# Performance work log

Hardware: AMD Instinct MI355X
Metric: run time of the kernel (lower is better)

The kernel has to match this reference:

```python
import jax, jax.numpy as jnp
import numpy as np

N_NODES = 307
U = 100          # gru units / GAT out dim
D_IN = 3         # per-node input features
F_IN = U + D_IN  # 103, GATv2 input dim
NEG_SLOPE = 0.2


def setup_inputs() -> dict:
    key = jax.random.key(0)
    ks = jax.random.split(key, 12)
    B, E = 256, 4096
    inputs = jax.random.normal(ks[0], (B, N_NODES * D_IN), dtype=jnp.float32)
    state = jax.random.normal(ks[1], (B, N_NODES * U), dtype=jnp.float32)
    src = jax.random.randint(ks[2], (E,), 0, N_NODES, dtype=jnp.int32)
    dst = jax.random.randint(ks[3], (E,), 0, N_NODES, dtype=jnp.int32)
    def glorot(k, shape):
        lim = float(np.sqrt(6.0 / (shape[0] + shape[1])))
        return jax.random.uniform(k, shape, jnp.float32, -lim, lim)
    return {
        "inputs": inputs, "state": state, "src": src, "dst": dst,
        "Wl": glorot(ks[4], (F_IN, U)),        # GATv2 lin_l (source)
        "Wr": glorot(ks[5], (F_IN, U)),        # GATv2 lin_r (target)
        "att": jax.random.normal(ks[6], (U,), jnp.float32) * 0.1,
        "gat_bias": jnp.zeros((U,), jnp.float32),
        "bias_gc": jnp.zeros((U,), jnp.float32),   # self.bias_1 added in _gc3
        "W_gru1": glorot(ks[7], (F_IN, 2 * U)),    # GRULinear(100,200)
        "b_gru1": jnp.zeros((2 * U,), jnp.float32),
        "W_gru2": glorot(ks[8], (F_IN, U)),        # GRULinear(100,100)
        "b_gru2": jnp.zeros((U,), jnp.float32),
    }


def _gru_linear(inputs, hidden, W, b):
    # cat((inputs[B,N,3], hidden[B,N,U]), -1) @ W + b
    B = hidden.shape[0]
    x = jnp.concatenate([inputs.reshape(B, N_NODES, D_IN),
                         hidden.reshape(B, N_NODES, U)], axis=2)
    return jnp.einsum('bnf,fo->bno', x, W) + b


def _gatv2(x, src, dst, Wl, Wr, att, gat_bias):
    # x: (B, N, F_IN); PyG GATv2Conv with heads=1, add_self_loops=True
    loops = jnp.arange(N_NODES, dtype=src.dtype)
    s = jnp.concatenate([src, loops])
    d = jnp.concatenate([dst, loops])
    xl = jnp.einsum('bnf,fu->bnu', x, Wl)  # source transform
    xr = jnp.einsum('bnf,fu->bnu', x, Wr)  # target transform

    def per_sample(xl_b, xr_b):
        m = xl_b[s]                                        # (E', U)
        e = jax.nn.leaky_relu(m + xr_b[d], NEG_SLOPE) @ att  # (E',)
        emax = jax.ops.segment_max(e, d, num_segments=N_NODES)
        ex = jnp.exp(e - emax[d])
        denom = jax.ops.segment_sum(ex, d, num_segments=N_NODES)
        alpha = ex / denom[d]
        return jax.ops.segment_sum(alpha[:, None] * m, d, num_segments=N_NODES)

    out = jax.vmap(per_sample)(xl, xr)  # (B, N, U)
    return out + gat_bias


def reference(inputs, state, src, dst, Wl, Wr, att, gat_bias, bias_gc,
              W_gru1, b_gru1, W_gru2, b_gru2):
    B = state.shape[0]
    # _gc3: cat([state, inputs]) -> GATv2 per sample -> + bias_1
    x = jnp.concatenate([state.reshape(B, N_NODES, U),
                         inputs.reshape(B, N_NODES, D_IN)], axis=2)
    st = _gatv2(x, src, dst, Wl, Wr, att, gat_bias) + bias_gc
    st = st.reshape(B, N_NODES * U)
    # GRU gating
    value = jax.nn.sigmoid(_gru_linear(inputs, st, W_gru1, b_gru1))  # (B,N,2U)
    r, u = jnp.split(value, 2, axis=-1)
    r = r.reshape(B, N_NODES * U)
    u = u.reshape(B, N_NODES * U)
    c = jnp.tanh(_gru_linear(inputs, r * st, W_gru2, b_gru2)).reshape(B, N_NODES * U)
    return u * st + (1.0 - u) * c
```

## Files before the change

kernel.cpp:

```cpp
#include <hip/hip_runtime.h>
#include <math.h>

#define NN 307
#define UU 100
#define DD 3
#define UP 104
#define UNIT_W 14336
#define HCAP 2560
#define NT 512
#define NGRP (NT / 16)

typedef _Float16 f16;
typedef f16  f16x2 __attribute__((ext_vector_type(2)));
typedef f16  f16x4 __attribute__((ext_vector_type(4)));
typedef f16  f16x8 __attribute__((ext_vector_type(8)));
typedef float f32x4 __attribute__((ext_vector_type(4)));
typedef unsigned short u16;

__global__ __launch_bounds__(256)
void pack_w_k(const float* __restrict__ Wl, const float* __restrict__ Wr,
              const float* __restrict__ Wg1, const float* __restrict__ Wg2,
              f16* __restrict__ Wp)
{
    const int idx = blockIdx.x * 256 + threadIdx.x;
    const int u   = idx / UNIT_W;
    const int rem = idx - u * UNIT_W;
    const int e   = rem & 7;
    const int l   = (rem >> 3) & 63;
    const int sj  = rem >> 9;
    const int s   = sj / 7, j = sj - 7 * s;
    const int col = j * 16 + (l & 15);
    const int k   = (s * 4 + (l >> 4)) * 8 + e;
    float v = 0.f;
    if (col < UU && k < UU + DD) {
        if (u == 0)      v = Wl[k * UU + col];
        else if (u == 1) v = Wr[k * UU + col];
        else {
            const int kk = (k < UU) ? (k + DD) : (k - UU);
            if (u == 2)      v = Wg1[kk * (2 * UU) + col];
            else if (u == 3) v = Wg1[kk * (2 * UU) + UU + col];
            else             v = Wg2[kk * UU + col];
        }
    }
    Wp[idx] = (f16)v;
}

__global__ __launch_bounds__(64)
void csr_count_k(const int* __restrict__ dst, int E, int* offs)
{
    const int d = blockIdx.x;
    const int lane = threadIdx.x;
    const int Etot = E + NN;
    int c = 0;
    for (int base = 0; base < Etot; base += 64) {
        const int e = base + lane;
        if (e < Etot) {
            const int de = (e < E) ? dst[e] : (e - E);
            c += (de == d) ? 1 : 0;
        }
    }
    #pragma unroll
    for (int m = 1; m < 64; m <<= 1) c += __shfl_xor(c, m, 64);
    if (lane == 0) {
        offs[d + 1] = c;
        if (d == 0) offs[0] = 0;
    }
}

__global__ __launch_bounds__(512)
void csr_scan_k(int* offs)
{
    __shared__ int c[512];
    const int t = threadIdx.x;
    c[t] = (t < NN) ? offs[t + 1] : 0;
    __syncthreads();
    #pragma unroll
    for (int off = 1; off < 512; off <<= 1) {
        const int v = (t >= off) ? c[t - off] : 0;
        __syncthreads();
        c[t] += v;
        __syncthreads();
    }
    if (t < NN) offs[t + 1] = c[t];
    if (t == 0) offs[0] = 0;
}

__global__ __launch_bounds__(64)
void csr_fill_k(const int* __restrict__ src, const int* __restrict__ dst,
                int E, const int* __restrict__ offs,
                int* eidx, int* ddst)
{
    const int d = blockIdx.x;
    const int lane = threadIdx.x;
    const int Etot = E + NN;
    int w = offs[d];
    for (int base = 0; base < Etot; base += 64) {
        const int e = base + lane;
        bool match = false;
        int se = 0;
        if (e < Etot) {
            const int de = (e < E) ? dst[e] : (e - E);
            se           = (e < E) ? src[e] : (e - E);
            match = (de == d);
        }
        const unsigned long long mask = __ballot(match);
        if (match) {
            const int pos = w + __popcll(mask & ((1ULL << lane) - 1ULL));
            eidx[pos] = se;
            ddst[pos] = d;
        }
        w += __popcll(mask);
    }
}

__device__ __forceinline__ void mma_unit_nb(const f16x8 (&af)[4],
                                            const f16* __restrict__ Wu,
                                            int l, f32x4 (&acc)[7])
{
    #pragma unroll
    for (int s = 0; s < 4; ++s)
        #pragma unroll
        for (int j = 0; j < 7; ++j) {
            const f16x8 bv = *(const f16x8*)(Wu + (((s * 7 + j) * 64 + l) << 3));
            acc[j] = __builtin_amdgcn_mfma_f32_16x16x32_f16(af[s], bv, acc[j], 0, 0, 0);
        }
}

__device__ __forceinline__ void z7(f32x4 (&acc)[7])
{
    #pragma unroll
    for (int j = 0; j < 7; ++j) acc[j] = (f32x4)0.f;
}

__device__ __forceinline__ float fast_sigmoid(float x)
{
    return __fdividef(1.f, 1.f + __expf(-x));
}

__device__ __forceinline__ float fast_tanh(float x)
{
    return 1.f - __fdividef(2.f, __expf(2.f * x) + 1.f);
}

__global__ __launch_bounds__(256, 4)
void gemm_xlxr_k(const float* __restrict__ state, const float* __restrict__ inp,
                 const f16* __restrict__ Wp,
                 f16* __restrict__ xl, f16* __restrict__ xr, int M)
{
    const int tid = threadIdx.x;
    const int w = tid >> 6, l = tid & 63, lr = l & 15, lk = l >> 4;
    const int rb = blockIdx.x * 64 + w * 16;
    int crow = rb + lr; if (crow >= M) crow = M - 1;
    const float* bf = state + (size_t)crow * UU;

    f16x8 af[4];
    #pragma unroll
    for (int s = 0; s < 3; ++s) {
        const int kb = s * 4 + lk;
        const float4 x0 = *(const float4*)(bf + kb * 8);
        const float4 x1 = *(const float4*)(bf + kb * 8 + 4);
        f16x8 v;
        v[0]=(f16)x0.x; v[1]=(f16)x0.y; v[2]=(f16)x0.z; v[3]=(f16)x0.w;
        v[4]=(f16)x1.x; v[5]=(f16)x1.y; v[6]=(f16)x1.z; v[7]=(f16)x1.w;
        af[s] = v;
    }
    {
        f16x8 v = (f16x8)(f16)0.f;
        if (lk == 0) {
            const float4 x0 = *(const float4*)(bf + 96);
            v[0]=(f16)x0.x; v[1]=(f16)x0.y; v[2]=(f16)x0.z; v[3]=(f16)x0.w;
            v[4] = (f16)inp[(size_t)crow * DD + 0];
            v[5] = (f16)inp[(size_t)crow * DD + 1];
            v[6] = (f16)inp[(size_t)crow * DD + 2];
            v[7] = (f16)0.f;
        }
        af[3] = v;
    }

    #pragma unroll
    for (int u = 0; u < 2; ++u) {
        f32x4 acc[7];
        z7(acc);
        mma_unit_nb(af, Wp + (size_t)u * UNIT_W, l, acc);
        f16* dst = u ? xr : xl;
        #pragma unroll
        for (int j = 0; j < 7; ++j) {
            const int col = j * 16 + lr;
            if (col >= UU) continue;
            #pragma unroll
            for (int r = 0; r < 4; ++r) {
                const int row = rb + lk * 4 + r;
                if (row < M) dst[(size_t)row * UP + col] = (f16)acc[j][r];
            }
        }
    }
}

__global__ __launch_bounds__(NT)
__attribute__((amdgpu_waves_per_eu(4, 4)))
void gat2h_k(const f16* __restrict__ xl, const f16* __restrict__ xr,
             const int* __restrict__ offs, const int* __restrict__ eidx,
             const int* __restrict__ ddst,
             const float* __restrict__ att, const float* __restrict__ gb,
             const float* __restrict__ bgc,
             f16* __restrict__ stg)
{
    __shared__ f16   xl_s[NN * UP];
    __shared__ float sc_s[HCAP];
    __shared__ u16   ei_s[HCAP];
    __shared__ f16   att_s[UP];

    const int b   = blockIdx.x;
    const int h   = blockIdx.y;
    const int tid = threadIdx.x;
    const int d0 = h * 154;
    const int d1 = (h == 0) ? 154 : NN;
    const f16* xlb = xl + (size_t)b * NN * UP;
    const f16* xrb = xr + (size_t)b * NN * UP;
    f16* stb = stg + (size_t)b * NN * UP;

    if (tid < UP) att_s[tid] = (tid < UU) ? (f16)att[tid] : (f16)0.f;
    for (int c = tid; c < NN * UP / 8; c += NT)
        *(f16x8*)&xl_s[c * 8] = *(const f16x8*)&xlb[c * 8];

    int dlo = d0;
    while (dlo < d1) {
        int dhi = d1;
        const int base = offs[dlo];
        if (offs[d1] - base > HCAP) {
            int lo = dlo + 1, hi = d1;
            while (lo < hi) {
                const int mid = (lo + hi + 1) >> 1;
                if (offs[mid] - base <= HCAP) lo = mid; else hi = mid - 1;
            }
            dhi = lo;
        }
        const int e0 = base, e1 = offs[dhi];
        const int n  = e1 - e0;

        for (int q = tid; q < n; q += NT) ei_s[q] = (u16)eidx[e0 + q];
        __syncthreads();

        for (int i = tid; i < n; i += NT) {
            const int s = ei_s[i];
            const int d = ddst[e0 + i];
            const f16x8* a8 = (const f16x8*)&xl_s[s * UP];
            const f16x8* r8 = (const f16x8*)(xrb + (size_t)d * UP);
            float p0 = 0.f, p1 = 0.f;
            #pragma unroll 4
            for (int c = 0; c < 13; ++c) {
                const f16x8 x  = a8[c] + r8[c];
                const f16x8 xm = x * (f16)0.2f;
                const f16x8 y  = __builtin_elementwise_max(x, xm);
                const f16x2* y2  = (const f16x2*)&y;
                const f16x2* at2 = (const f16x2*)&att_s[c * 8];
#if __has_builtin(__builtin_amdgcn_fdot2)
                p0 = __builtin_amdgcn_fdot2(y2[0], at2[0], p0, false);
                p1 = __builtin_amdgcn_fdot2(y2[1], at2[1], p1, false);
                p0 = __builtin_amdgcn_fdot2(y2[2], at2[2], p0, false);
                p1 = __builtin_amdgcn_fdot2(y2[3], at2[3], p1, false);
#else
                #pragma unroll
                for (int q = 0; q < 4; ++q) {
                    p0 += (float)y2[q][0] * (float)at2[q][0];
                    p1 += (float)y2[q][1] * (float)at2[q][1];
                }
#endif
            }
            sc_s[i] = p0 + p1;
        }
        __syncthreads();

        {
            const int t = dlo + tid;
            if (t < dhi) {
                const int f0 = offs[t] - e0, f1 = offs[t + 1] - e0;
                float mx = -1e30f;
                for (int e = f0; e < f1; ++e) mx = fmaxf(mx, sc_s[e]);
                float dn = 0.f;
                for (int e = f0; e < f1; ++e) {
                    const float ex = __expf(sc_s[e] - mx);
                    sc_s[e] = ex;
                    dn += ex;
                }
                const float inv = 1.f / dn;
                for (int e = f0; e < f1; ++e) sc_s[e] *= inv;
            }
        }
        __syncthreads();

        {
            const int g   = tid >> 4;
            const int sub = tid & 15;
            const bool fa = (sub < 13);
            float bias_r[8];
            #pragma unroll
            for (int k = 0; k < 8; ++k) {
                const int f = sub * 8 + k;
                bias_r[k] = (fa && f < UU) ? (gb[f] + bgc[f]) : 0.f;
            }
            for (int d = dlo + g; d < dhi; d += NGRP) {
                const int f0 = offs[d] - e0, f1 = offs[d + 1] - e0;
                float acc[8] = {0.f, 0.f, 0.f, 0.f, 0.f, 0.f, 0.f, 0.f};
                for (int e = f0; e < f1; ++e) {
                    const float alpha = sc_s[e];
                    const int s = ei_s[e];
                    if (fa) {
                        const f16x8 m = *(const f16x8*)&xl_s[s * UP + sub * 8];
                        #pragma unroll
                        for (int k = 0; k < 8; ++k) acc[k] += alpha * (float)m[k];
                    }
                }
                if (fa) {
                    f16x8 o;
                    #pragma unroll
                    for (int k = 0; k < 8; ++k) o[k] = (f16)(acc[k] + bias_r[k]);
                    *(f16x8*)(stb + (size_t)d * UP + sub * 8) = o;
                }
            }
        }
        dlo = dhi;
        __syncthreads();
    }
}

__global__ __launch_bounds__(256, 4)
void gru3_k(const f16* __restrict__ st, const float* __restrict__ inp,
            const f16* __restrict__ Wp2 ,
            const float* __restrict__ bg1, const float* __restrict__ bg2,
            float* __restrict__ out, int M)
{
    __shared__ f16 st_s[64 * UP];
    __shared__ f16 rst_s[64 * UP];

    const int tid = threadIdx.x;
    const int w = tid >> 6, l = tid & 63, lr = l & 15, lk = l >> 4;
    const int rb = blockIdx.x * 64 + w * 16;
    const int lbase = w * 16;

    #pragma unroll
    for (int p = 0; p < 4; ++p) {
        const int idx = p * 64 + l;
        const int row = idx >> 4, ch = idx & 15;
        if (ch < 13) {
            int gr = rb + row; if (gr >= M) gr = M - 1;
            *(f16x8*)&st_s[(lbase + row) * UP + ch * 8] =
                *(const f16x8*)(st + (size_t)gr * UP + ch * 8);
        }
    }

    int crow = rb + lr; if (crow >= M) crow = M - 1;
    const f16* bh = &st_s[(lbase + lr) * UP];
    f16x8 af[4];
    #pragma unroll
    for (int s = 0; s < 3; ++s)
        af[s] = *(const f16x8*)(bh + (s * 4 + lk) * 8);
    {
        f16x8 v = (f16x8)(f16)0.f;
        if (lk == 0) {
            v = *(const f16x8*)(bh + 96);
            v[4] = (f16)inp[(size_t)crow * DD + 0];
            v[5] = (f16)inp[(size_t)crow * DD + 1];
            v[6] = (f16)inp[(size_t)crow * DD + 2];
            v[7] = (f16)0.f;
        }
        af[3] = v;
    }

    f32x4 acc[7];

    z7(acc);
    mma_unit_nb(af, Wp2, l, acc);
    #pragma unroll
    for (int j = 0; j < 7; ++j) {
        const int col = j * 16 + lr;
        if (col >= UU) continue;
        const float bR = bg1[col];
        #pragma unroll
        for (int r = 0; r < 4; ++r) {
            const int grow = rb + lk * 4 + r;
            const int lrow = lbase + lk * 4 + r;
            if (grow < M) {
                const float stv = (float)st_s[lrow * UP + col];
                const float sg = fast_sigmoid(acc[j][r] + bR);
                rst_s[lrow * UP + col] = (f16)(sg * stv);
            }
        }
    }
    if (l < 16) {
        const int grow2 = rb + l;
        const int lrow2 = lbase + l;
        if (grow2 < M) {
            rst_s[lrow2 * UP + 100] = (f16)inp[(size_t)grow2 * DD + 0];
            rst_s[lrow2 * UP + 101] = (f16)inp[(size_t)grow2 * DD + 1];
            rst_s[lrow2 * UP + 102] = (f16)inp[(size_t)grow2 * DD + 2];
            rst_s[lrow2 * UP + 103] = (f16)0.f;
        }
    }

    z7(acc);
    mma_unit_nb(af, Wp2 + UNIT_W, l, acc);
    f16x4 uh[7];
    #pragma unroll
    for (int j = 0; j < 7; ++j) {
        const int col = j * 16 + lr;
        const float bU = (col < UU) ? bg1[UU + col] : 0.f;
        #pragma unroll
        for (int r = 0; r < 4; ++r)
            uh[j][r] = (f16)fast_sigmoid(acc[j][r] + bU);
    }

    f16x8 af2[4];
    #pragma unroll
    for (int s = 0; s < 3; ++s)
        af2[s] = *(const f16x8*)&rst_s[(lbase + lr) * UP + (s * 4 + lk) * 8];
    af2[3] = (lk == 0) ? *(const f16x8*)&rst_s[(lbase + lr) * UP + 96]
                       : (f16x8)(f16)0.f;

    z7(acc);
    mma_unit_nb(af2, Wp2 + 2 * UNIT_W, l, acc);
    #pragma unroll
    for (int j = 0; j < 7; ++j) {
        const int col = j * 16 + lr;
        if (col >= UU) continue;
        const float bC = bg2[col];
        #pragma unroll
        for (int r = 0; r < 4; ++r) {
            const int grow = rb + lk * 4 + r;
            const int lrow = lbase + lk * 4 + r;
            if (grow < M) {
                const float c = fast_tanh(acc[j][r] + bC);
                const float u = (float)uh[j][r];
                const float stv = (float)st_s[lrow * UP + col];
                out[(size_t)grow * UU + col] = u * stv + (1.f - u) * c;
            }
        }
    }
}

extern "C" void kernel_launch(void* const* d_in, const int* in_sizes, int n_in,
                              void* d_out, int out_size, void* d_ws, size_t ws_size,
                              hipStream_t stream)
{
    const float* inputs   = (const float*)d_in[0];
    const float* state    = (const float*)d_in[1];
    const int*   src      = (const int*)  d_in[2];
    const int*   dst      = (const int*)  d_in[3];
    const float* Wl       = (const float*)d_in[4];
    const float* Wr       = (const float*)d_in[5];
    const float* att      = (const float*)d_in[6];
    const float* gat_bias = (const float*)d_in[7];
    const float* bias_gc  = (const float*)d_in[8];
    const float* Wg1      = (const float*)d_in[9];
    const float* bg1      = (const float*)d_in[10];
    const float* Wg2      = (const float*)d_in[11];
    const float* bg2      = (const float*)d_in[12];

    const int E = in_sizes[2];
    const int B = in_sizes[1] / (NN * UU);
    const int M = B * NN;
    const int Etot = E + NN;

    char* ws = (char*)d_ws;
    f16* Wp   = (f16*)ws;
    int* offs = (int*)(ws + 5 * UNIT_W * sizeof(f16));
    int* eidx = offs + (NN + 1);
    int* ddst = eidx + (Etot + 64);
    f16* xl_h = (f16*)(ws + (256 << 10));
    f16* xr_h = xl_h + (size_t)M * UP;
    f16* st_h = xr_h + (size_t)M * UP;
    float* out = (float*)d_out;

    pack_w_k<<<280, 256, 0, stream>>>(Wl, Wr, Wg1, Wg2, Wp);
    csr_count_k<<<NN, 64, 0, stream>>>(dst, E, offs);
    csr_scan_k<<<1, 512, 0, stream>>>(offs);
    csr_fill_k<<<NN, 64, 0, stream>>>(src, dst, E, offs, eidx, ddst);

    gemm_xlxr_k<<<(M + 63) / 64, 256, 0, stream>>>(state, inputs, Wp,
                                                   xl_h, xr_h, M);

    gat2h_k<<<dim3(B, 2), NT, 0, stream>>>(xl_h, xr_h, offs, eidx, ddst,
                                           att, gat_bias, bias_gc, st_h);

    gru3_k<<<(M + 63) / 64, 256, 0, stream>>>(st_h, inputs,
        Wp + 2 * (size_t)UNIT_W, bg1, bg2, out, M);
}
```

Before: 156.0 us.

## Fuse GATv2 aggregation with GRU gating in one kernel via shared memory

Merges the GAT attention/aggregation kernel and the GRU MFMA kernel into a single kernel per (batch, half-node-range) block. When a block's edges fit in shared memory, the aggregated node states are kept in LDS, reusing the xl buffer, and consumed directly by the three GRU matmuls, avoiding a global round trip of the intermediate state and one launch. A fallback path keeps the old chunked loop and reads the state from global memory. The fused kernel runs the GRU tiles with 8 waves over 154 nodes, so some waves idle, and it adds register pressure from holding five accumulator rows per thread.

```diff
diff --git a/kernel.cpp b/kernel.cpp
--- a/kernel.cpp
+++ b/kernel.cpp
@@ -198,12 +198,14 @@
 
 __global__ __launch_bounds__(NT)
 __attribute__((amdgpu_waves_per_eu(4, 4)))
-void gat2h_k(const f16* __restrict__ xl, const f16* __restrict__ xr,
-             const int* __restrict__ offs, const int* __restrict__ eidx,
-             const int* __restrict__ ddst,
-             const float* __restrict__ att, const float* __restrict__ gb,
-             const float* __restrict__ bgc,
-             f16* __restrict__ stg)
+void gatgru_k(const f16* __restrict__ xl, const f16* __restrict__ xr,
+              const int* __restrict__ offs, const int* __restrict__ eidx,
+              const int* __restrict__ ddst,
+              const float* __restrict__ att, const float* __restrict__ gb,
+              const float* __restrict__ bgc,
+              const float* __restrict__ inputs, const f16* __restrict__ Wp2,
+              const float* __restrict__ bg1, const float* __restrict__ bg2,
+              f16* __restrict__ stg, float* __restrict__ out)
 {
     __shared__ f16   xl_s[NN * UP];
     __shared__ float sc_s[HCAP];
@@ -213,31 +215,26 @@
     const int b   = blockIdx.x;
     const int h   = blockIdx.y;
     const int tid = threadIdx.x;
+    const int w = tid >> 6, l = tid & 63, lr = l & 15, lk = l >> 4;
     const int d0 = h * 154;
     const int d1 = (h == 0) ? 154 : NN;
     const f16* xlb = xl + (size_t)b * NN * UP;
     const f16* xrb = xr + (size_t)b * NN * UP;
+    const float* inb = inputs + (size_t)b * NN * DD;
     f16* stb = stg + (size_t)b * NN * UP;
+
+    f16* st_s  = xl_s;
+    f16* rst_s = xl_s + 160 * UP;
 
     if (tid < UP) att_s[tid] = (tid < UU) ? (f16)att[tid] : (f16)0.f;
     for (int c = tid; c < NN * UP / 8; c += NT)
         *(f16x8*)&xl_s[c * 8] = *(const f16x8*)&xlb[c * 8];
 
-    int dlo = d0;
-    while (dlo < d1) {
-        int dhi = d1;
-        const int base = offs[dlo];
-        if (offs[d1] - base > HCAP) {
-            int lo = dlo + 1, hi = d1;
-            while (lo < hi) {
-                const int mid = (lo + hi + 1) >> 1;
-                if (offs[mid] - base <= HCAP) lo = mid; else hi = mid - 1;
-            }
-            dhi = lo;
-        }
-        const int e0 = base, e1 = offs[dhi];
-        const int n  = e1 - e0;
-
+    const bool fits = (offs[d1] - offs[d0]) <= HCAP;
+
+    if (fits) {
+        const int e0 = offs[d0];
+        const int n  = offs[d1] - e0;
         for (int q = tid; q < n; q += NT) ei_s[q] = (u16)eidx[e0 + q];
         __syncthreads();
 
@@ -272,8 +269,8 @@
         __syncthreads();
 
         {
-            const int t = dlo + tid;
-            if (t < dhi) {
+            const int t = d0 + tid;
+            if (t < d1) {
                 const int f0 = offs[t] - e0, f1 = offs[t + 1] - e0;
                 float mx = -1e30f;
                 for (int e = f0; e < f1; ++e) mx = fmaxf(mx, sc_s[e]);
@@ -289,150 +286,223 @@
         }
         __syncthreads();
 
+        const int g   = tid >> 4;
+        const int sub = tid & 15;
+        const bool fa = (sub < 13);
+        float acc2[5][8];
+        #pragma unroll
+        for (int dd = 0; dd < 5; ++dd)
+            #pragma unroll
+            for (int k = 0; k < 8; ++k) acc2[dd][k] = 0.f;
+        #pragma unroll
+        for (int dd = 0; dd < 5; ++dd) {
+            const int d = d0 + g + dd * NGRP;
+            if (d < d1 && fa) {
+                const int f0 = offs[d] - e0, f1 = offs[d + 1] - e0;
+                for (int e = f0; e < f1; ++e) {
+                    const float alpha = sc_s[e];
+                    const int s = ei_s[e];
+                    const f16x8 m = *(const f16x8*)&xl_s[s * UP + sub * 8];
+                    #pragma unroll
+                    for (int k = 0; k < 8; ++k) acc2[dd][k] += alpha * (float)m[k];
+                }
+            }
+        }
+        __syncthreads();
+
         {
-            const int g   = tid >> 4;
-            const int sub = tid & 15;
-            const bool fa = (sub < 13);
             float bias_r[8];
             #pragma unroll
             for (int k = 0; k < 8; ++k) {
                 const int f = sub * 8 + k;
                 bias_r[k] = (fa && f < UU) ? (gb[f] + bgc[f]) : 0.f;
             }
-            for (int d = dlo + g; d < dhi; d += NGRP) {
-                const int f0 = offs[d] - e0, f1 = offs[d + 1] - e0;
-                float acc[8] = {0.f, 0.f, 0.f, 0.f, 0.f, 0.f, 0.f, 0.f};
-                for (int e = f0; e < f1; ++e) {
-                    const float alpha = sc_s[e];
-                    const int s = ei_s[e];
-                    if (fa) {
-                        const f16x8 m = *(const f16x8*)&xl_s[s * UP + sub * 8];
-                        #pragma unroll
-                        for (int k = 0; k < 8; ++k) acc[k] += alpha * (float)m[k];
-                    }
-                }
-                if (fa) {
+            #pragma unroll
+            for (int dd = 0; dd < 5; ++dd) {
+                const int d = d0 + g + dd * NGRP;
+                if (d < d1 && fa) {
                     f16x8 o;
                     #pragma unroll
-                    for (int k = 0; k < 8; ++k) o[k] = (f16)(acc[k] + bias_r[k]);
-                    *(f16x8*)(stb + (size_t)d * UP + sub * 8) = o;
-                }
-            }
-        }
-        dlo = dhi;
-        __syncthreads();
-    }
-}
-
-__global__ __launch_bounds__(256, 4)
-void gru3_k(const f16* __restrict__ st, const float* __restrict__ inp,
-            const f16* __restrict__ Wp2 ,
-            const float* __restrict__ bg1, const float* __restrict__ bg2,
-            float* __restrict__ out, int M)
-{
-    __shared__ f16 st_s[64 * UP];
-    __shared__ f16 rst_s[64 * UP];
-
-    const int tid = threadIdx.x;
-    const int w = tid >> 6, l = tid & 63, lr = l & 15, lk = l >> 4;
-    const int rb = blockIdx.x * 64 + w * 16;
-    const int lbase = w * 16;
-
-    #pragma unroll
-    for (int p = 0; p < 4; ++p) {
-        const int idx = p * 64 + l;
-        const int row = idx >> 4, ch = idx & 15;
-        if (ch < 13) {
-            int gr = rb + row; if (gr >= M) gr = M - 1;
-            *(f16x8*)&st_s[(lbase + row) * UP + ch * 8] =
-                *(const f16x8*)(st + (size_t)gr * UP + ch * 8);
-        }
-    }
-
-    int crow = rb + lr; if (crow >= M) crow = M - 1;
-    const f16* bh = &st_s[(lbase + lr) * UP];
-    f16x8 af[4];
-    #pragma unroll
-    for (int s = 0; s < 3; ++s)
-        af[s] = *(const f16x8*)(bh + (s * 4 + lk) * 8);
-    {
-        f16x8 v = (f16x8)(f16)0.f;
-        if (lk == 0) {
-            v = *(const f16x8*)(bh + 96);
-            v[4] = (f16)inp[(size_t)crow * DD + 0];
-            v[5] = (f16)inp[(size_t)crow * DD + 1];
-            v[6] = (f16)inp[(size_t)crow * DD + 2];
-            v[7] = (f16)0.f;
-        }
-        af[3] = v;
-    }
-
-    f32x4 acc[7];
-
-    z7(acc);
-    mma_unit_nb(af, Wp2, l, acc);
-    #pragma unroll
-    for (int j = 0; j < 7; ++j) {
-        const int col = j * 16 + lr;
-        if (col >= UU) continue;
-        const float bR = bg1[col];
-        #pragma unroll
-        for (int r = 0; r < 4; ++r) {
-            const int grow = rb + lk * 4 + r;
-            const int lrow = lbase + lk * 4 + r;
-            if (grow < M) {
-                const float stv = (float)st_s[lrow * UP + col];
-                const float sg = fast_sigmoid(acc[j][r] + bR);
-                rst_s[lrow * UP + col] = (f16)(sg * stv);
-            }
-        }
-    }
-    if (l < 16) {
-        const int grow2 = rb + l;
-        const int lrow2 = lbase + l;
-        if (grow2 < M) {
-            rst_s[lrow2 * UP + 100] = (f16)inp[(size_t)grow2 * DD + 0];
-            rst_s[lrow2 * UP + 101] = (f16)inp[(size_t)grow2 * DD + 1];
-            rst_s[lrow2 * UP + 102] = (f16)inp[(size_t)grow2 * DD + 2];
-            rst_s[lrow2 * UP + 103] = (f16)0.f;
-        }
-    }
-
-    z7(acc);
-    mma_unit_nb(af, Wp2 + UNIT_W, l, acc);
-    f16x4 uh[7];
-    #pragma unroll
-    for (int j = 0; j < 7; ++j) {
-        const int col = j * 16 + lr;
-        const float bU = (col < UU) ? bg1[UU + col] : 0.f;
-        #pragma unroll
-        for (int r = 0; r < 4; ++r)
-            uh[j][r] = (f16)fast_sigmoid(acc[j][r] + bU);
-    }
-
-    f16x8 af2[4];
-    #pragma unroll
-    for (int s = 0; s < 3; ++s)
-        af2[s] = *(const f16x8*)&rst_s[(lbase + lr) * UP + (s * 4 + lk) * 8];
-    af2[3] = (lk == 0) ? *(const f16x8*)&rst_s[(lbase + lr) * UP + 96]
-                       : (f16x8)(f16)0.f;
-
-    z7(acc);
-    mma_unit_nb(af2, Wp2 + 2 * UNIT_W, l, acc);
-    #pragma unroll
-    for (int j = 0; j < 7; ++j) {
-        const int col = j * 16 + lr;
-        if (col >= UU) continue;
-        const float bC = bg2[col];
-        #pragma unroll
-        for (int r = 0; r < 4; ++r) {
-            const int grow = rb + lk * 4 + r;
-            const int lrow = lbase + lk * 4 + r;
-            if (grow < M) {
-                const float c = fast_tanh(acc[j][r] + bC);
-                const float u = (float)uh[j][r];
-                const float stv = (float)st_s[lrow * UP + col];
-                out[(size_t)grow * UU + col] = u * stv + (1.f - u) * c;
+                    for (int k = 0; k < 8; ++k) o[k] = (f16)(acc2[dd][k] + bias_r[k]);
+                    *(f16x8*)&st_s[(d - d0) * UP + sub * 8] = o;
+                }
+            }
+        }
+        __syncthreads();
+    } else {
+        int dlo = d0;
+        while (dlo < d1) {
+            int dhi = d1;
+            const int base = offs[dlo];
+            if (offs[d1] - base > HCAP) {
+                int lo = dlo + 1, hi = d1;
+                while (lo < hi) {
+                    const int mid = (lo + hi + 1) >> 1;
+                    if (offs[mid] - base <= HCAP) lo = mid; else hi = mid - 1;
+                }
+                dhi = lo;
+            }
+            const int e0 = base;
+            const int n  = offs[dhi] - e0;
+            for (int q = tid; q < n; q += NT) ei_s[q] = (u16)eidx[e0 + q];
+            __syncthreads();
+            for (int i = tid; i < n; i += NT) {
+                const int s = ei_s[i];
+                const int d = ddst[e0 + i];
+                const f16x8* a8 = (const f16x8*)&xl_s[s * UP];
+                const f16x8* r8 = (const f16x8*)(xrb + (size_t)d * UP);
+                float p0 = 0.f, p1 = 0.f;
+                #pragma unroll 4
+                for (int c = 0; c < 13; ++c) {
+                    const f16x8 x  = a8[c] + r8[c];
+                    const f16x8 xm = x * (f16)0.2f;
+                    const f16x8 y  = __builtin_elementwise_max(x, xm);
+                    #pragma unroll
+                    for (int q = 0; q < 8; ++q)
+                        ((q & 1) ? p1 : p0) += (float)y[q] * (float)att_s[c * 8 + q];
+                }
+                sc_s[i] = p0 + p1;
+            }
+            __syncthreads();
+            {
+                const int t = dlo + tid;
+                if (t < dhi) {
+                    const int f0 = offs[t] - e0, f1 = offs[t + 1] - e0;
+                    float mx = -1e30f;
+                    for (int e = f0; e < f1; ++e) mx = fmaxf(mx, sc_s[e]);
+                    float dn = 0.f;
+                    for (int e = f0; e < f1; ++e) {
+                        const float ex = __expf(sc_s[e] - mx);
+                        sc_s[e] = ex; dn += ex;
+                    }
+                    const float inv = 1.f / dn;
+                    for (int e = f0; e < f1; ++e) sc_s[e] *= inv;
+                }
+            }
+            __syncthreads();
+            {
+                const int g   = tid >> 4;
+                const int sub = tid & 15;
+                const bool fa = (sub < 13);
+                float bias_r[8];
+                #pragma unroll
+                for (int k = 0; k < 8; ++k) {
+                    const int f = sub * 8 + k;
+                    bias_r[k] = (fa && f < UU) ? (gb[f] + bgc[f]) : 0.f;
+                }
+                for (int d = dlo + g; d < dhi; d += NGRP) {
+                    const int f0 = offs[d] - e0, f1 = offs[d + 1] - e0;
+                    float acc[8] = {0,0,0,0,0,0,0,0};
+                    for (int e = f0; e < f1; ++e) {
+                        const float alpha = sc_s[e];
+                        const int s = ei_s[e];
+                        if (fa) {
+                            const f16x8 m = *(const f16x8*)&xl_s[s * UP + sub * 8];
+                            #pragma unroll
+                            for (int k = 0; k < 8; ++k) acc[k] += alpha * (float)m[k];
+                        }
+                    }
+                    if (fa) {
+                        f16x8 o;
+                        #pragma unroll
+                        for (int k = 0; k < 8; ++k) o[k] = (f16)(acc[k] + bias_r[k]);
+                        *(f16x8*)(stb + (size_t)d * UP + sub * 8) = o;
+                    }
+                }
+            }
+            dlo = dhi;
+            __syncthreads();
+        }
+    }
+
+    const int nt = (d1 - d0 + 15) >> 4;
+    for (int tile = w; tile < nt; tile += 8) {
+        const int node0 = d0 + tile * 16;
+        int crow = node0 + lr; if (crow >= d1) crow = d1 - 1;
+        const f16* bh = fits ? &st_s[(crow - d0) * UP]
+                             : (stb + (size_t)crow * UP);
+        f16x8 af[4];
+        #pragma unroll
+        for (int s = 0; s < 3; ++s)
+            af[s] = *(const f16x8*)(bh + (s * 4 + lk) * 8);
+        {
+            f16x8 v = (f16x8)(f16)0.f;
+            if (lk == 0) {
+                v = *(const f16x8*)(bh + 96);
+                v[4] = (f16)inb[(size_t)crow * DD + 0];
+                v[5] = (f16)inb[(size_t)crow * DD + 1];
+                v[6] = (f16)inb[(size_t)crow * DD + 2];
+                v[7] = (f16)0.f;
+            }
+            af[3] = v;
+        }
+
+        f32x4 acc[7];
+
+        z7(acc);
+        mma_unit_nb(af, Wp2, l, acc);
+        #pragma unroll
+        for (int j = 0; j < 7; ++j) {
+            const int col = j * 16 + lr;
+            if (col >= UU) continue;
+            const float bR = bg1[col];
+            #pragma unroll
+            for (int r = 0; r < 4; ++r) {
+                const int node = node0 + lk * 4 + r;
+                if (node < d1) {
+                    const float stv = fits ? (float)st_s[(node - d0) * UP + col]
+                                           : (float)stb[(size_t)node * UP + col];
+                    const float sg = fast_sigmoid(acc[j][r] + bR);
+                    rst_s[(w * 16 + lk * 4 + r) * UP + col] = (f16)(sg * stv);
+                }
+            }
+        }
+        if (l < 16) {
+            const int node2 = node0 + l;
+            if (node2 < d1) {
+                rst_s[(w * 16 + l) * UP + 100] = (f16)inb[(size_t)node2 * DD + 0];
+                rst_s[(w * 16 + l) * UP + 101] = (f16)inb[(size_t)node2 * DD + 1];
+                rst_s[(w * 16 + l) * UP + 102] = (f16)inb[(size_t)node2 * DD + 2];
+                rst_s[(w * 16 + l) * UP + 103] = (f16)0.f;
+            }
+        }
+
+        z7(acc);
+        mma_unit_nb(af, Wp2 + UNIT_W, l, acc);
+        f16x4 uh[7];
+        #pragma unroll
+        for (int j = 0; j < 7; ++j) {
+            const int col = j * 16 + lr;
+            const float bU = (col < UU) ? bg1[UU + col] : 0.f;
+            #pragma unroll
+            for (int r = 0; r < 4; ++r)
+                uh[j][r] = (f16)fast_sigmoid(acc[j][r] + bU);
+        }
+
+        f16x8 af2[4];
+        #pragma unroll
+        for (int s = 0; s < 3; ++s)
+            af2[s] = *(const f16x8*)&rst_s[(w * 16 + lr) * UP + (s * 4 + lk) * 8];
+        af2[3] = (lk == 0) ? *(const f16x8*)&rst_s[(w * 16 + lr) * UP + 96]
+                           : (f16x8)(f16)0.f;
+
+        z7(acc);
+        mma_unit_nb(af2, Wp2 + 2 * UNIT_W, l, acc);
+        #pragma unroll
+        for (int j = 0; j < 7; ++j) {
+            const int col = j * 16 + lr;
+            if (col >= UU) continue;
+            const float bC = bg2[col];
+            #pragma unroll
+            for (int r = 0; r < 4; ++r) {
+                const int node = node0 + lk * 4 + r;
+                if (node < d1) {
+                    const float c = fast_tanh(acc[j][r] + bC);
+                    const float u = (float)uh[j][r];
+                    const float stv = fits ? (float)st_s[(node - d0) * UP + col]
+                                           : (float)stb[(size_t)node * UP + col];
+                    out[((size_t)b * NN + node) * UU + col] = u * stv + (1.f - u) * c;
+                }
             }
         }
     }
@@ -479,9 +549,7 @@
     gemm_xlxr_k<<<(M + 63) / 64, 256, 0, stream>>>(state, inputs, Wp,
                                                    xl_h, xr_h, M);
 
-    gat2h_k<<<dim3(B, 2), NT, 0, stream>>>(xl_h, xr_h, offs, eidx, ddst,
-                                           att, gat_bias, bias_gc, st_h);
-
-    gru3_k<<<(M + 63) / 64, 256, 0, stream>>>(st_h, inputs,
-        Wp + 2 * (size_t)UNIT_W, bg1, bg2, out, M);
-}
+    gatgru_k<<<dim3(B, 2), NT, 0, stream>>>(xl_h, xr_h, offs, eidx, ddst,
+        att, gat_bias, bias_gc, inputs, Wp + 2 * (size_t)UNIT_W,
+        bg1, bg2, st_h, out);
+}
```

Result: slower. 350.1 us (+124.4%).
